# Kernel tuning notes

Measured on AMD Instinct MI355X. Metric: run time of the kernel, lower is better.

## Reference

```python
import jax, jax.numpy as jnp
import numpy as np

DECAY = 0.99
EPS = 1e-05
NUM_EMBEDDINGS = 2048
EMBEDDING_DIM = 512


def setup_inputs() -> dict:
    key = jax.random.key(0)
    k1, k2 = jax.random.split(key)
    z_e = jax.random.normal(k1, (16, 4096, EMBEDDING_DIM), dtype=jnp.float32)
    embedding = jax.random.normal(k2, (NUM_EMBEDDINGS, EMBEDDING_DIM), dtype=jnp.float32)
    cluster_size = jnp.zeros((NUM_EMBEDDINGS,), dtype=jnp.float32)
    embed_avg = embedding  # buffer initialized as a clone of embedding
    return {"z_e": z_e, "embedding": embedding, "cluster_size": cluster_size, "embed_avg": embed_avg}


def reference(z_e, embedding, cluster_size, embed_avg):
    K, D = embedding.shape
    flat = z_e.reshape(-1, D)  # [N, D]
    dist = (jnp.sum(flat * flat, axis=1, keepdims=True)
            - 2.0 * flat @ embedding.T
            + jnp.sum(embedding * embedding, axis=1))
    idx = jnp.argmin(dist, axis=1)  # [N] int
    z_q_raw = embedding[idx].reshape(z_e.shape)

    # EMA cluster statistics (training path). one_hot.T @ flat == segment_sum
    counts = jax.ops.segment_sum(jnp.ones_like(idx, dtype=flat.dtype), idx, num_segments=K)
    embed_sum = jax.ops.segment_sum(flat, idx, num_segments=K)  # [K, D]
    new_cluster_size = DECAY * cluster_size + (1.0 - DECAY) * counts
    new_embed_avg = DECAY * embed_avg + (1.0 - DECAY) * embed_sum
    n = jnp.sum(new_cluster_size)
    cs_smoothed = (new_cluster_size + EPS) / (n + K * EPS) * n
    new_embedding = new_embed_avg / cs_smoothed[:, None]

    # straight-through estimator
    z_q = z_e + jax.lax.stop_gradient(z_q_raw - z_e)
    commit_loss = jnp.mean((jax.lax.stop_gradient(z_e) - z_q) ** 2)
    codebook_loss = jnp.mean((z_e - jax.lax.stop_gradient(z_q)) ** 2)
    vq_loss = codebook_loss + 0.25 * commit_loss
    return (z_q, idx, vq_loss, new_embedding, new_cluster_size, new_embed_avg)
```

## Files before the change

### kernel.cpp

```cpp
#include <hip/hip_runtime.h>

typedef unsigned short ushort_t;
typedef unsigned int u32;
typedef unsigned long long u64;
typedef __attribute__((ext_vector_type(8))) short bf16x8;
typedef __attribute__((ext_vector_type(4))) float f32x4;

#define N_ROWS 65536
#define K_EMB  2048
#define D_DIM  512
#define OFF_ZQ   0
#define OFF_IDX  33554432
#define OFF_LOSS 33619968
#define OFF_EMB  33619969
#define OFF_NCS  34668545
#define OFF_NEA  34670593
#define TAU 1.5f
#define CHUNK 128
#define MAXCHUNK 2560

__device__ __forceinline__ ushort_t f2bf(float f) {
  u32 u = __float_as_uint(f);
  u32 r = (u + 0x7fffu + ((u >> 16) & 1u)) >> 16;
  return (ushort_t)r;
}
__device__ __forceinline__ void glds16(const void* g, void* l) {
  __builtin_amdgcn_global_load_lds((const __attribute__((address_space(1))) u32*)g,
                                   (__attribute__((address_space(3))) u32*)l, 16, 0, 0);
}

#define MERGE4(s1,s2,s3,s4,o1,o2,o3,o4) do {                        \
    u32 x1 = min(s1,o4), x2 = min(s2,o3), x3 = min(s3,o2), x4 = min(s4,o1); \
    u32 t1 = min(x1,x3), t3 = max(x1,x3), t2 = min(x2,x4), t4 = max(x2,x4); \
    s1 = min(t1,t2); s2 = max(t1,t2); s3 = min(t3,t4); s4 = max(t3,t4);     \
  } while (0)

__global__ void prep_kernel(const float* __restrict__ ze, const float* __restrict__ emb,
                            ushort_t* __restrict__ xh, ushort_t* __restrict__ eh,
                            float* __restrict__ enorm, float* __restrict__ counts,
                            float* __restrict__ lossws)
{
  int bx = blockIdx.x;
  int t = threadIdx.x;
  if (bx < 512) {
    int w = t >> 6, l = t & 63;
    int k = bx * 4 + w;
    const float4* row = (const float4*)(emb + (size_t)k * D_DIM);
    float4 a = row[l * 2], b = row[l * 2 + 1];
    ushort4 h0, h1;
    h0.x = f2bf(a.x); h0.y = f2bf(a.y); h0.z = f2bf(a.z); h0.w = f2bf(a.w);
    h1.x = f2bf(b.x); h1.y = f2bf(b.y); h1.z = f2bf(b.z); h1.w = f2bf(b.w);
    ((ushort4*)(eh + (size_t)k * D_DIM))[l * 2] = h0;
    ((ushort4*)(eh + (size_t)k * D_DIM))[l * 2 + 1] = h1;
    float s = a.x*a.x + a.y*a.y + a.z*a.z + a.w*a.w + b.x*b.x + b.y*b.y + b.z*b.z + b.w*b.w;
    #pragma unroll
    for (int off = 32; off >= 1; off >>= 1) s += __shfl_xor(s, off);
    if (l == 0) enorm[k] = s;
  } else {
    int gid = (bx - 512) * 256 + t;
    const float4* zin = (const float4*)ze;
    ushort4* xh4 = (ushort4*)xh;
    for (int g = gid; g < (N_ROWS * D_DIM / 4); g += 8192 * 256) {
      float4 v = zin[g];
      ushort4 h;
      h.x = f2bf(v.x); h.y = f2bf(v.y); h.z = f2bf(v.z); h.w = f2bf(v.w);
      xh4[g] = h;
    }
    if (gid < K_EMB) counts[gid] = 0.0f;
    if (gid == 0) lossws[0] = 0.0f;
  }
}

__global__ __launch_bounds__(256, 2)
void dist_gemm(const ushort_t* __restrict__ xh, const ushort_t* __restrict__ eh,
               const float* __restrict__ enorm, uint4* __restrict__ list)
{
  __shared__ ushort_t Ah[2][128 * 64];
  __shared__ ushort_t Bh[2][128 * 64];
  const int t = threadIdx.x;
  const int w = t >> 6, l = t & 63;
  const int li = l & 15, lg = l >> 4;
  const int row0 = blockIdx.x << 7;
  const int wr = (w >> 1) << 6, wc = (w & 1) << 6;

  u32 cand[16][4];
  #pragma unroll
  for (int mi = 0; mi < 16; ++mi) {
    cand[mi][0] = 0xFFFFFFFFu; cand[mi][1] = 0xFFFFFFFFu;
    cand[mi][2] = 0xFFFFFFFFu; cand[mi][3] = 0xFFFFFFFFu;
  }

  f32x4 acc[4][4];
  #pragma unroll
  for (int m = 0; m < 4; ++m)
    #pragma unroll
    for (int n = 0; n < 4; ++n) acc[m][n] = (f32x4){0.f, 0.f, 0.f, 0.f};

  const int Gbase = (w << 6) + l;

#define STAGE(buf_, s_) do {                                                   \
    int kb_ = ((s_) & 7) << 7;                                                 \
    int c0_ = ((s_) >> 3) << 7;                                                \
    _Pragma("unroll")                                                          \
    for (int i = 0; i < 4; ++i) {                                              \
      int G = (i << 8) + Gbase;                           \
      int r = G >> 3, gp = G & 7;                                              \
      int cb = gp ^ (r & 7);                          \
      size_t gA = ((size_t)(row0 + r) << 10) + kb_ + (cb << 4);                \
      size_t gB = ((size_t)(c0_ + r) << 10) + kb_ + (cb << 4);                 \
      int ld = ((i << 8) + (w << 6)) << 4;              \
      glds16((const char*)xh + gA, (char*)Ah[buf_] + ld);                      \
      glds16((const char*)eh + gB, (char*)Bh[buf_] + ld);                      \
    }                                                                          \
  } while (0)

  STAGE(0, 0);
  __syncthreads();
  int buf = 0;
  float en0 = 0.f, en1 = 0.f, en2 = 0.f, en3 = 0.f;

  for (int s = 0; s < 128; ++s) {
    if ((s & 7) == 0) {
      int col0 = (s >> 3) << 7;
      en0 = enorm[col0 + wc + 0  + li];
      en1 = enorm[col0 + wc + 16 + li];
      en2 = enorm[col0 + wc + 32 + li];
      en3 = enorm[col0 + wc + 48 + li];
    }
    if (s != 127) STAGE(buf ^ 1, s + 1);

    #pragma unroll
    for (int kblk = 0; kblk < 2; ++kblk) {
      bf16x8 fah[4], fbh[4];
      #pragma unroll
      for (int m = 0; m < 4; ++m) {
        int r = wr + (m << 4) + li;
        int c = (kblk << 2) + lg;
        int off = (r << 7) + ((c ^ (r & 7)) << 4);
        fah[m] = *(const bf16x8*)((const char*)Ah[buf] + off);
      }
      #pragma unroll
      for (int n = 0; n < 4; ++n) {
        int r = wc + (n << 4) + li;
        int c = (kblk << 2) + lg;
        int off = (r << 7) + ((c ^ (r & 7)) << 4);
        fbh[n] = *(const bf16x8*)((const char*)Bh[buf] + off);
      }
      #pragma unroll
      for (int m = 0; m < 4; ++m)
        #pragma unroll
        for (int n = 0; n < 4; ++n)
          acc[m][n] = __builtin_amdgcn_mfma_f32_16x16x32_bf16(fah[m], fbh[n], acc[m][n], 0, 0, 0);
    }

    if ((s & 7) == 7) {
      int col0 = (s >> 3) << 7;
      const u32 colb = (u32)(col0 + wc + li);
      #pragma unroll
      for (int m = 0; m < 4; ++m)
        #pragma unroll
        for (int i = 0; i < 4; ++i) {
          u32 k0 = (__float_as_uint(fmaf(-2.f, acc[m][0][i], en0)) & 0xFFFFF800u) | colb;
          u32 k1 = (__float_as_uint(fmaf(-2.f, acc[m][1][i], en1)) & 0xFFFFF800u) | (colb + 16u);
          u32 k2 = (__float_as_uint(fmaf(-2.f, acc[m][2][i], en2)) & 0xFFFFF800u) | (colb + 32u);
          u32 k3 = (__float_as_uint(fmaf(-2.f, acc[m][3][i], en3)) & 0xFFFFF800u) | (colb + 48u);
          u32 a = min(k0, k1), b = max(k0, k1);
          u32 c = min(k2, k3), d = max(k2, k3);
          u32 e = min(a, c),  f = max(a, c);
          u32 g = min(b, d),  h = max(b, d);
          u32 q1 = e, q2 = min(f, g), q3 = max(f, g), q4 = h;
          MERGE4(cand[m * 4 + i][0], cand[m * 4 + i][1],
                 cand[m * 4 + i][2], cand[m * 4 + i][3], q1, q2, q3, q4);
          acc[m][0][i] = 0.f; acc[m][1][i] = 0.f;
          acc[m][2][i] = 0.f; acc[m][3][i] = 0.f;
        }
    }
    __syncthreads();
    buf ^= 1;
  }
#undef STAGE

  #pragma unroll
  for (int mi = 0; mi < 16; ++mi) {
    u32 s1 = cand[mi][0], s2 = cand[mi][1], s3 = cand[mi][2], s4 = cand[mi][3];
    #pragma unroll
    for (int off = 1; off <= 8; off <<= 1) {
      u32 o1 = __shfl_xor(s1, off), o2 = __shfl_xor(s2, off);
      u32 o3 = __shfl_xor(s3, off), o4 = __shfl_xor(s4, off);
      MERGE4(s1, s2, s3, s4, o1, o2, o3, o4);
    }
    cand[mi][0] = s1; cand[mi][1] = s2; cand[mi][2] = s3; cand[mi][3] = s4;
  }

  u32* ex = (u32*)Ah;
  if ((w & 1) == 1 && li == 0) {
    #pragma unroll
    for (int m = 0; m < 4; ++m)
      #pragma unroll
      for (int i = 0; i < 4; ++i) {
        int lrow = wr + (m << 4) + (lg << 2) + i;
        uint4 v;
        v.x = cand[m * 4 + i][0]; v.y = cand[m * 4 + i][1];
        v.z = cand[m * 4 + i][2]; v.w = cand[m * 4 + i][3];
        *(uint4*)&ex[lrow << 2] = v;
      }
  }
  __syncthreads();
  if ((w & 1) == 0 && li == 0) {
    #pragma unroll
    for (int m = 0; m < 4; ++m)
      #pragma unroll
      for (int i = 0; i < 4; ++i) {
        int lrow = wr + (m << 4) + (lg << 2) + i;
        const u32* p = &ex[lrow << 2];
        u32 s1 = cand[m * 4 + i][0], s2 = cand[m * 4 + i][1];
        u32 s3 = cand[m * 4 + i][2], s4 = cand[m * 4 + i][3];
        u32 o1 = p[0], o2 = p[1], o3 = p[2], o4 = p[3];
        MERGE4(s1, s2, s3, s4, o1, o2, o3, o4);
        uint4 v; v.x = s1; v.y = s2; v.z = s3; v.w = s4;
        list[row0 + lrow] = v;
      }
  }
}

__global__ void finalize_kernel(const uint4* __restrict__ list, const float* __restrict__ ze,
                                const float* __restrict__ emb, int* __restrict__ wsidx,
                                float* __restrict__ counts)
{
  int w = threadIdx.x >> 6, l = threadIdx.x & 63;
  int row = blockIdx.x * 4 + w;
  uint4 q = list[row];
  float d1 = __uint_as_float(q.x & 0xFFFFF800u);
  float lim = d1 + TAU;
  bool n2 = (q.y != 0xFFFFFFFFu) && (__uint_as_float(q.y & 0xFFFFF800u) < lim);
  bool n3 = (q.z != 0xFFFFFFFFu) && (__uint_as_float(q.z & 0xFFFFF800u) < lim);
  bool n4 = (q.w != 0xFFFFFFFFu) && (__uint_as_float(q.w & 0xFFFFF800u) < lim);
  int idx;
  if (!(n2 | n3 | n4)) {
    idx = (int)(q.x & 2047u);
  } else {
    double bd = 1e300; int bc = 0x7fffffff;
    const float* xr = ze + (((size_t)row) << 9);
    double xv[8];
    #pragma unroll
    for (int p = 0; p < 8; ++p) xv[p] = (double)xr[(l << 3) + p];
    #pragma unroll
    for (int j = 0; j < 4; ++j) {
      u32 kj = (j == 0) ? q.x : (j == 1) ? q.y : (j == 2) ? q.z : q.w;
      bool ok = (j == 0) || ((kj != 0xFFFFFFFFu) &&
                             (__uint_as_float(kj & 0xFFFFF800u) < lim));
      if (!ok) continue;
      int col = (int)(kj & 2047u);
      const float* er = emb + (((size_t)col) << 9);
      double s = 0.0;
      #pragma unroll
      for (int p = 0; p < 8; ++p) {
        double df = xv[p] - (double)er[(l << 3) + p];
        s += df * df;
      }
      #pragma unroll
      for (int off = 32; off >= 1; off >>= 1) s += __shfl_xor(s, off);
      if (s < bd || (s == bd && col < bc)) { bd = s; bc = col; }
    }
    idx = bc;
  }
  if (l == 0) {
    wsidx[row] = idx;
    atomicAdd(&counts[idx], 1.0f);
  }
}

__global__ void scan_kernel(const float* __restrict__ counts, u32* __restrict__ offsets,
                            u32* __restrict__ cursor, u32* __restrict__ chunkinfo,
                            u32* __restrict__ ntotal)
{
  int t = threadIdx.x;
  int c[8]; int s = 0;
  #pragma unroll
  for (int i = 0; i < 8; ++i) { c[i] = (int)counts[t * 8 + i]; s += c[i]; }
  __shared__ int ts[256];
  ts[t] = s; __syncthreads();
  for (int off = 1; off < 256; off <<= 1) {
    int v = (t >= off) ? ts[t - off] : 0;
    __syncthreads();
    ts[t] += v;
    __syncthreads();
  }
  int run = ts[t] - s;
  int nch[8]; int ns = 0;
  #pragma unroll
  for (int i = 0; i < 8; ++i) {
    offsets[t * 8 + i] = (u32)run;
    cursor[t * 8 + i] = 0;
    run += c[i];
    nch[i] = (c[i] + CHUNK - 1) / CHUNK;
    ns += nch[i];
  }
  __shared__ int ts2[256];
  ts2[t] = ns; __syncthreads();
  for (int off = 1; off < 256; off <<= 1) {
    int v = (t >= off) ? ts2[t - off] : 0;
    __syncthreads();
    ts2[t] += v;
    __syncthreads();
  }
  int cb = ts2[t] - ns;
  #pragma unroll
  for (int i = 0; i < 8; ++i)
    for (int cc = 0; cc < nch[i]; ++cc)
      chunkinfo[cb++] = (u32)(t * 8 + i) | ((u32)cc << 11);
  if (t == 255) *ntotal = (u32)ts2[255];
}

__global__ void scatter_kernel(const int* __restrict__ wsidx, const u32* __restrict__ offsets,
                               u32* __restrict__ cursor, u32* __restrict__ sorted)
{
  int row = blockIdx.x * 256 + threadIdx.x;
  int idx = wsidx[row];
  u32 pos = atomicAdd(&cursor[idx], 1u);
  sorted[offsets[idx] + pos] = (u32)row;
}

__global__ void zesum_kernel(const float* __restrict__ counts, float* __restrict__ esum)
{
  int k = blockIdx.x;
  float c = counts[k];
  if (c == 0.0f || c > (float)CHUNK) {
    esum[((size_t)k << 9) + threadIdx.x] = 0.0f;
    esum[((size_t)k << 9) + 256 + threadIdx.x] = 0.0f;
  }
}

__global__ __launch_bounds__(256)
void zq_seg_kernel(const float* __restrict__ ze, const float* __restrict__ emb,
                   const u32* __restrict__ offsets, const float* __restrict__ counts,
                   const u32* __restrict__ sorted, const u32* __restrict__ chunkinfo,
                   const u32* __restrict__ ntotal, float* __restrict__ o_zq,
                   float* __restrict__ o_idx, float* __restrict__ esum,
                   float* __restrict__ lossws)
{
  int cid = blockIdx.x;
  if (cid >= (int)*ntotal) return;
  u32 rec = chunkinfo[cid];
  int k = rec & 2047, c = (int)(rec >> 11);
  int ctotal = (int)counts[k];
  int base = (int)offsets[k] + c * CHUNK;
  int cnt = min(ctotal - c * CHUNK, CHUNK);
  bool multi = ctotal > CHUNK;
  int t = threadIdx.x, w = t >> 6, l = t & 63;
  __shared__ u32 srow[CHUNK];
  __shared__ float sacc[4 * 512];
  __shared__ float sloss[4];
  if (t < cnt) srow[t] = sorted[base + t];
  __syncthreads();
  const float4* e4 = (const float4*)(emb + ((size_t)k << 9));
  float4 ev0 = e4[l * 2], ev1 = e4[l * 2 + 1];
  float a0x=0,a0y=0,a0z=0,a0w=0,a1x=0,a1y=0,a1z=0,a1w=0;
  float lacc = 0.f;
  for (int r = w; r < cnt; r += 4) {
    int row = (int)srow[r];
    const float4* z4 = (const float4*)(ze + ((size_t)row << 9));
    float4 zv0 = z4[l * 2], zv1 = z4[l * 2 + 1];
    float4 q0, q1;
    q0.x = zv0.x + (ev0.x - zv0.x);
    q0.y = zv0.y + (ev0.y - zv0.y);
    q0.z = zv0.z + (ev0.z - zv0.z);
    q0.w = zv0.w + (ev0.w - zv0.w);
    q1.x = zv1.x + (ev1.x - zv1.x);
    q1.y = zv1.y + (ev1.y - zv1.y);
    q1.z = zv1.z + (ev1.z - zv1.z);
    q1.w = zv1.w + (ev1.w - zv1.w);
    float4* zq4 = (float4*)(o_zq + ((size_t)row << 9));
    zq4[l * 2] = q0; zq4[l * 2 + 1] = q1;
    float dx = zv0.x - q0.x, dy = zv0.y - q0.y, dz = zv0.z - q0.z, dw = zv0.w - q0.w;
    lacc += dx*dx + dy*dy + dz*dz + dw*dw;
    dx = zv1.x - q1.x; dy = zv1.y - q1.y; dz = zv1.z - q1.z; dw = zv1.w - q1.w;
    lacc += dx*dx + dy*dy + dz*dz + dw*dw;
    a0x += zv0.x; a0y += zv0.y; a0z += zv0.z; a0w += zv0.w;
    a1x += zv1.x; a1y += zv1.y; a1z += zv1.z; a1w += zv1.w;
    if (l == 0) o_idx[row] = (float)k;
  }
  #pragma unroll
  for (int off = 32; off >= 1; off >>= 1) lacc += __shfl_xor(lacc, off);
  if (l == 0) sloss[w] = lacc;
  float* sa = sacc + w * 512 + l * 8;
  sa[0]=a0x; sa[1]=a0y; sa[2]=a0z; sa[3]=a0w; sa[4]=a1x; sa[5]=a1y; sa[6]=a1z; sa[7]=a1w;
  __syncthreads();
  #pragma unroll
  for (int j = 0; j < 2; ++j) {
    int col = t * 2 + j;
    float v = sacc[col] + sacc[512 + col] + sacc[1024 + col] + sacc[1536 + col];
    if (multi) atomicAdd(&esum[((size_t)k << 9) + col], v);
    else       esum[((size_t)k << 9) + col] = v;
  }
  if (t == 0) atomicAdd(lossws, sloss[0] + sloss[1] + sloss[2] + sloss[3]);
}

__global__ void d1_kernel(const float* __restrict__ cs, const float* __restrict__ counts,
                          float* __restrict__ o_ncs, float* __restrict__ inv,
                          const float* __restrict__ lossws, float* __restrict__ o_loss)
{
  int t = threadIdx.x;
  float ncs[8]; float s = 0.0f;
  #pragma unroll
  for (int i = 0; i < 8; ++i) {
    int k = t + (i << 8);
    float v = 0.99f * cs[k] + 0.01f * counts[k];
    ncs[i] = v; o_ncs[k] = v; s += v;
  }
  __shared__ float red[256];
  red[t] = s; __syncthreads();
  for (int h = 128; h >= 1; h >>= 1) { if (t < h) red[t] += red[t + h]; __syncthreads(); }
  float n = red[0];
  float denom = n + 2048.0f * 1e-5f;
  #pragma unroll
  for (int i = 0; i < 8; ++i) {
    int k = t + (i << 8);
    float sm = (ncs[i] + 1e-5f) / denom * n;
    inv[k] = 1.0f / sm;
  }
  if (t == 0) o_loss[0] = lossws[0] * 1.25f / 33554432.0f;
}

__global__ void d2_kernel(const float* __restrict__ ea, const float* __restrict__ inv,
                          float* __restrict__ o_emb, float* __restrict__ o_nea)
{
  int gid = blockIdx.x * 256 + threadIdx.x;
  for (int i = gid; i < K_EMB * D_DIM; i += 1024 * 256) {
    float es = o_emb[i];
    float nea = 0.99f * ea[i] + 0.01f * es;
    o_nea[i] = nea;
    o_emb[i] = nea * inv[i >> 9];
  }
}

extern "C" void kernel_launch(void* const* d_in, const int* in_sizes, int n_in,
                              void* d_out, int out_size, void* d_ws, size_t ws_size,
                              hipStream_t stream)
{
  const float* ze  = (const float*)d_in[0];
  const float* emb = (const float*)d_in[1];
  const float* cs  = (const float*)d_in[2];
  const float* ea  = (const float*)d_in[3];
  float* out = (float*)d_out;
  float* o_zq   = out + OFF_ZQ;
  float* o_idx  = out + OFF_IDX;
  float* o_loss = out + OFF_LOSS;
  float* o_emb  = out + OFF_EMB;
  float* o_ncs  = out + OFF_NCS;
  float* o_nea  = out + OFF_NEA;
  ushort_t* xh = (ushort_t*)d_out;
  char* ws = (char*)d_ws;
  ushort_t* ehp = (ushort_t*)ws;
  int* wsidx    = (int*)(ws + 2097152);
  float* counts = (float*)(ws + 2097152 + 262144);
  float* enorm  = counts + 2048;
  float* inv    = enorm + 2048;
  float* lossws = inv + 2048;
  u32* offsets  = (u32*)(lossws + 64);
  u32* cursor   = offsets + 2048;
  u32* sorted   = cursor + 2048;
  u32* chunkinfo= sorted + 65536;
  u32* ntotal   = chunkinfo + MAXCHUNK;
  uint4* list   = (uint4*)(ws + 3145728);

  prep_kernel<<<8704, 256, 0, stream>>>(ze, emb, xh, ehp, enorm, counts, lossws);
  dist_gemm<<<512, 256, 0, stream>>>(xh, ehp, enorm, list);
  finalize_kernel<<<16384, 256, 0, stream>>>(list, ze, emb, wsidx, counts);
  scan_kernel<<<1, 256, 0, stream>>>(counts, offsets, cursor, chunkinfo, ntotal);
  scatter_kernel<<<256, 256, 0, stream>>>(wsidx, offsets, cursor, sorted);
  zesum_kernel<<<2048, 256, 0, stream>>>(counts, o_emb);
  zq_seg_kernel<<<MAXCHUNK, 256, 0, stream>>>(ze, emb, offsets, counts, sorted,
                                              chunkinfo, ntotal, o_zq, o_idx, o_emb, lossws);
  d1_kernel<<<1, 256, 0, stream>>>(cs, counts, o_ncs, inv, lossws, o_loss);
  d2_kernel<<<1024, 256, 0, stream>>>(ea, inv, o_emb, o_nea);
}
```

Measured before the change: 343.7 us.

## Fuse EMA update into segment kernel and merge small tail kernels

Folds the cluster-size EMA and inverse computation into the scan kernel, and merges the scatter and zeroing kernels into one launch. For codes with a single chunk, the embed_avg EMA and the normalised embedding are written directly from the segment-sum kernel. A per-code tail kernel then handles only the empty and multi-chunk codes, which removes a full pass over the 2048x512 buffers and two launches. Index output moves into finalize. The cost is a heavier single-block scan kernel and more branching.

New measurement: 335.4 us. 1.02x faster.

```diff
diff --git a/kernel.cpp b/kernel.cpp
--- a/kernel.cpp
+++ b/kernel.cpp
@@ -225,7 +225,7 @@
 
 __global__ void finalize_kernel(const uint4* __restrict__ list, const float* __restrict__ ze,
                                 const float* __restrict__ emb, int* __restrict__ wsidx,
-                                float* __restrict__ counts)
+                                float* __restrict__ counts, float* __restrict__ o_idx)
 {
   int w = threadIdx.x >> 6, l = threadIdx.x & 63;
   int row = blockIdx.x * 4 + w;
@@ -266,25 +266,43 @@
   }
   if (l == 0) {
     wsidx[row] = idx;
+    o_idx[row] = (float)idx;
     atomicAdd(&counts[idx], 1.0f);
   }
 }
 
-__global__ void scan_kernel(const float* __restrict__ counts, u32* __restrict__ offsets,
-                            u32* __restrict__ cursor, u32* __restrict__ chunkinfo,
-                            u32* __restrict__ ntotal)
+__global__ void scan_kernel(const float* __restrict__ counts, const float* __restrict__ cs,
+                            u32* __restrict__ offsets, u32* __restrict__ cursor,
+                            u32* __restrict__ chunkinfo, u32* __restrict__ ntotal,
+                            float* __restrict__ o_ncs, float* __restrict__ inv)
 {
   int t = threadIdx.x;
   int c[8]; int s = 0;
-  #pragma unroll
-  for (int i = 0; i < 8; ++i) { c[i] = (int)counts[t * 8 + i]; s += c[i]; }
+  float ncs[8]; float nsum = 0.0f;
+  #pragma unroll
+  for (int i = 0; i < 8; ++i) {
+    int k = t * 8 + i;
+    c[i] = (int)counts[k]; s += c[i];
+    float v = 0.99f * cs[k] + 0.01f * counts[k];
+    ncs[i] = v; o_ncs[k] = v; nsum += v;
+  }
   __shared__ int ts[256];
+  __shared__ float red[256];
+  red[t] = nsum;
   ts[t] = s; __syncthreads();
   for (int off = 1; off < 256; off <<= 1) {
     int v = (t >= off) ? ts[t - off] : 0;
     __syncthreads();
     ts[t] += v;
     __syncthreads();
+  }
+  for (int h = 128; h >= 1; h >>= 1) { if (t < h) red[t] += red[t + h]; __syncthreads(); }
+  float n = red[0];
+  float denom = n + 2048.0f * 1e-5f;
+  #pragma unroll
+  for (int i = 0; i < 8; ++i) {
+    float sm = (ncs[i] + 1e-5f) / denom * n;
+    inv[t * 8 + i] = 1.0f / sm;
   }
   int run = ts[t] - s;
   int nch[8]; int ns = 0;
@@ -312,31 +330,34 @@
   if (t == 255) *ntotal = (u32)ts2[255];
 }
 
-__global__ void scatter_kernel(const int* __restrict__ wsidx, const u32* __restrict__ offsets,
-                               u32* __restrict__ cursor, u32* __restrict__ sorted)
-{
-  int row = blockIdx.x * 256 + threadIdx.x;
-  int idx = wsidx[row];
-  u32 pos = atomicAdd(&cursor[idx], 1u);
-  sorted[offsets[idx] + pos] = (u32)row;
-}
-
-__global__ void zesum_kernel(const float* __restrict__ counts, float* __restrict__ esum)
-{
-  int k = blockIdx.x;
-  float c = counts[k];
-  if (c == 0.0f || c > (float)CHUNK) {
-    esum[((size_t)k << 9) + threadIdx.x] = 0.0f;
-    esum[((size_t)k << 9) + 256 + threadIdx.x] = 0.0f;
+__global__ void scatter_zero_kernel(const int* __restrict__ wsidx, const u32* __restrict__ offsets,
+                                    u32* __restrict__ cursor, u32* __restrict__ sorted,
+                                    const float* __restrict__ counts, float* __restrict__ esum)
+{
+  int bx = blockIdx.x;
+  int t = threadIdx.x;
+  if (bx < 256) {
+    int row = bx * 256 + t;
+    int idx = wsidx[row];
+    u32 pos = atomicAdd(&cursor[idx], 1u);
+    sorted[offsets[idx] + pos] = (u32)row;
+  } else {
+    int k = bx - 256;
+    float c = counts[k];
+    if (c == 0.0f || c > (float)CHUNK) {
+      esum[((size_t)k << 9) + t] = 0.0f;
+      esum[((size_t)k << 9) + 256 + t] = 0.0f;
+    }
   }
 }
 
 __global__ __launch_bounds__(256)
 void zq_seg_kernel(const float* __restrict__ ze, const float* __restrict__ emb,
+                   const float* __restrict__ ea, const float* __restrict__ inv,
                    const u32* __restrict__ offsets, const float* __restrict__ counts,
                    const u32* __restrict__ sorted, const u32* __restrict__ chunkinfo,
                    const u32* __restrict__ ntotal, float* __restrict__ o_zq,
-                   float* __restrict__ o_idx, float* __restrict__ esum,
+                   float* __restrict__ esum, float* __restrict__ o_nea,
                    float* __restrict__ lossws)
 {
   int cid = blockIdx.x;
@@ -378,7 +399,6 @@
     lacc += dx*dx + dy*dy + dz*dz + dw*dw;
     a0x += zv0.x; a0y += zv0.y; a0z += zv0.z; a0w += zv0.w;
     a1x += zv1.x; a1y += zv1.y; a1z += zv1.z; a1w += zv1.w;
-    if (l == 0) o_idx[row] = (float)k;
   }
   #pragma unroll
   for (int off = 32; off >= 1; off >>= 1) lacc += __shfl_xor(lacc, off);
@@ -386,51 +406,42 @@
   float* sa = sacc + w * 512 + l * 8;
   sa[0]=a0x; sa[1]=a0y; sa[2]=a0z; sa[3]=a0w; sa[4]=a1x; sa[5]=a1y; sa[6]=a1z; sa[7]=a1w;
   __syncthreads();
+  float ikv = inv[k];
   #pragma unroll
   for (int j = 0; j < 2; ++j) {
     int col = t * 2 + j;
     float v = sacc[col] + sacc[512 + col] + sacc[1024 + col] + sacc[1536 + col];
-    if (multi) atomicAdd(&esum[((size_t)k << 9) + col], v);
-    else       esum[((size_t)k << 9) + col] = v;
+    if (multi) {
+      atomicAdd(&esum[((size_t)k << 9) + col], v);
+    } else {
+      float nea = 0.99f * ea[((size_t)k << 9) + col] + 0.01f * v;
+      o_nea[((size_t)k << 9) + col] = nea;
+      esum[((size_t)k << 9) + col] = nea * ikv;
+    }
   }
   if (t == 0) atomicAdd(lossws, sloss[0] + sloss[1] + sloss[2] + sloss[3]);
 }
 
-__global__ void d1_kernel(const float* __restrict__ cs, const float* __restrict__ counts,
-                          float* __restrict__ o_ncs, float* __restrict__ inv,
-                          const float* __restrict__ lossws, float* __restrict__ o_loss)
-{
+__global__ void tail_kernel(const float* __restrict__ counts, const float* __restrict__ ea,
+                            const float* __restrict__ inv, float* __restrict__ o_emb,
+                            float* __restrict__ o_nea, const float* __restrict__ lossws,
+                            float* __restrict__ o_loss)
+{
+  int k = blockIdx.x;
   int t = threadIdx.x;
-  float ncs[8]; float s = 0.0f;
-  #pragma unroll
-  for (int i = 0; i < 8; ++i) {
-    int k = t + (i << 8);
-    float v = 0.99f * cs[k] + 0.01f * counts[k];
-    ncs[i] = v; o_ncs[k] = v; s += v;
-  }
-  __shared__ float red[256];
-  red[t] = s; __syncthreads();
-  for (int h = 128; h >= 1; h >>= 1) { if (t < h) red[t] += red[t + h]; __syncthreads(); }
-  float n = red[0];
-  float denom = n + 2048.0f * 1e-5f;
-  #pragma unroll
-  for (int i = 0; i < 8; ++i) {
-    int k = t + (i << 8);
-    float sm = (ncs[i] + 1e-5f) / denom * n;
-    inv[k] = 1.0f / sm;
-  }
-  if (t == 0) o_loss[0] = lossws[0] * 1.25f / 33554432.0f;
-}
-
-__global__ void d2_kernel(const float* __restrict__ ea, const float* __restrict__ inv,
-                          float* __restrict__ o_emb, float* __restrict__ o_nea)
-{
-  int gid = blockIdx.x * 256 + threadIdx.x;
-  for (int i = gid; i < K_EMB * D_DIM; i += 1024 * 256) {
-    float es = o_emb[i];
-    float nea = 0.99f * ea[i] + 0.01f * es;
-    o_nea[i] = nea;
-    o_emb[i] = nea * inv[i >> 9];
+  if (k == 0 && t == 0) o_loss[0] = lossws[0] * 1.25f / 33554432.0f;
+  float c = counts[k];
+  bool empty = (c == 0.0f), multi = (c > (float)CHUNK);
+  if (!(empty | multi)) return;
+  float ikv = inv[k];
+  #pragma unroll
+  for (int j = 0; j < 2; ++j) {
+    int col = t + (j << 8);
+    size_t p = ((size_t)k << 9) + col;
+    float es = empty ? 0.0f : o_emb[p];
+    float nea = 0.99f * ea[p] + 0.01f * es;
+    o_nea[p] = nea;
+    o_emb[p] = nea * ikv;
   }
 }
 
@@ -466,12 +477,12 @@
 
   prep_kernel<<<8704, 256, 0, stream>>>(ze, emb, xh, ehp, enorm, counts, lossws);
   dist_gemm<<<512, 256, 0, stream>>>(xh, ehp, enorm, list);
-  finalize_kernel<<<16384, 256, 0, stream>>>(list, ze, emb, wsidx, counts);
-  scan_kernel<<<1, 256, 0, stream>>>(counts, offsets, cursor, chunkinfo, ntotal);
-  scatter_kernel<<<256, 256, 0, stream>>>(wsidx, offsets, cursor, sorted);
-  zesum_kernel<<<2048, 256, 0, stream>>>(counts, o_emb);
-  zq_seg_kernel<<<MAXCHUNK, 256, 0, stream>>>(ze, emb, offsets, counts, sorted,
-                                              chunkinfo, ntotal, o_zq, o_idx, o_emb, lossws);
-  d1_kernel<<<1, 256, 0, stream>>>(cs, counts, o_ncs, inv, lossws, o_loss);
-  d2_kernel<<<1024, 256, 0, stream>>>(ea, inv, o_emb, o_nea);
-}
+  finalize_kernel<<<16384, 256, 0, stream>>>(list, ze, emb, wsidx, counts, o_idx);
+  scan_kernel<<<1, 256, 0, stream>>>(counts, cs, offsets, cursor, chunkinfo, ntotal,
+                                     o_ncs, inv);
+  scatter_zero_kernel<<<2304, 256, 0, stream>>>(wsidx, offsets, cursor, sorted,
+                                                counts, o_emb);
+  zq_seg_kernel<<<MAXCHUNK, 256, 0, stream>>>(ze, emb, ea, inv, offsets, counts, sorted,
+                                              chunkinfo, ntotal, o_zq, o_emb, o_nea, lossws);
+  tail_kernel<<<2048, 256, 0, stream>>>(counts, ea, inv, o_emb, o_nea, lossws, o_loss);
+}
```
